# Optimization experiments

Hardware: AMD Instinct MI355X
Metric: run time of the kernel (lower is better)

The kernel has to match this reference:

```python
import jax, jax.numpy as jnp
import numpy as np

M = 16
WIDTH = 9 * M  # 144, hardcoded width_G=9 in original __init__
N_NODES = 100000
E = 1000000
DEPTH = 3


def setup_inputs() -> dict:
    key = jax.random.key(0)
    ks = jax.random.split(key, 16)
    inp = {}
    inp["score"] = jax.random.normal(ks[0], (N_NODES, 1), dtype=jnp.float32)
    inp["label_idx"] = jax.random.randint(ks[1], (E, 2 * M), 0, N_NODES, dtype=jnp.int64)
    s = 1.0 / np.sqrt(2 * M)
    inp["W_start"] = jax.random.uniform(ks[2], (2 * M, WIDTH), jnp.float32, -s, s)
    inp["b_start"] = jax.random.uniform(ks[3], (WIDTH,), jnp.float32, -s, s)
    sh = 1.0 / np.sqrt(WIDTH)
    for i in range(DEPTH):
        inp[f"W_h{i}"] = jax.random.uniform(ks[4 + 2 * i], (WIDTH, WIDTH), jnp.float32, -sh, sh)
        inp[f"b_h{i}"] = jax.random.uniform(ks[5 + 2 * i], (WIDTH,), jnp.float32, -sh, sh)
    inp["W_end"] = jax.random.uniform(ks[10], (WIDTH, 1), jnp.float32, -sh, sh)
    inp["b_end"] = jax.random.uniform(ks[11], (1,), jnp.float32, -sh, sh)
    return inp


def reference(score, label_idx, W_start, b_start, W_h0, b_h0, W_h1, b_h1, W_h2, b_h2, W_end, b_end):
    # Gather: score is [N,1]; score[label_idx] -> [E, 2M, 1] -> [E, 2M]
    node_input = score[label_idx, 0]  # [E, 2M]
    x = jax.nn.relu(node_input @ W_start + b_start)  # [E, 9M]
    for W, b in ((W_h0, b_h0), (W_h1, b_h1), (W_h2, b_h2)):
        x = jax.nn.relu(x @ W + b)
    return x @ W_end + b_end  # [E, 1]
```

## Files before the change

kernel.cpp:

```cpp
#include <hip/hip_runtime.h>

#define EPW 64
#define NTH 64
#define STRIDE 168

using f32x4 = __attribute__((ext_vector_type(4))) float;
using bf8   = __attribute__((ext_vector_type(8))) short;

__device__ __forceinline__ ushort f2bf(float f) {
    union { float f; unsigned u; } c{f};
    unsigned u = c.u;
    return (ushort)((u + 0x7fffu + ((u >> 16) & 1u)) >> 16);
}

__device__ __forceinline__ unsigned cvt_pk_bf16(float lo, float hi) {
    unsigned r;
    asm("v_cvt_pk_bf16_f32 %0, %1, %2" : "=v"(r) : "v"(lo), "v"(hi));
    return r;
}

__global__ void repack_kernel(const float* __restrict__ Wstart,
                              const float* __restrict__ Wh0,
                              const float* __restrict__ Wh1,
                              const float* __restrict__ Wh2,
                              ushort* __restrict__ frag) {
    int i = blockIdx.x * blockDim.x + threadIdx.x;
    if (i < 4608) {
        int j = i & 7, l = (i >> 3) & 63, nt = i >> 9;
        int k = ((l >> 4) << 3) + j;
        int n = nt * 16 + (l & 15);
        frag[i] = f2bf(Wstart[k * 144 + n]);
    } else if (i < 73728) {
        int r = i - 4608;
        int h = r / 23040; r %= 23040;
        const float* W = (h == 0) ? Wh0 : ((h == 1) ? Wh1 : Wh2);
        int j = r & 7, l = (r >> 3) & 63, rem = r >> 9;
        int ks = rem % 5, nt = rem / 5;
        int k = ks * 32 + ((l >> 4) << 3) + j;
        int n = nt * 16 + (l & 15);
        float v = (k < 144) ? W[k * 144 + n] : 0.0f;
        frag[i] = f2bf(v);
    }
}

template<int KS, bool FINAL>
__device__ __forceinline__ void layer_w(const ushort* __restrict__ wfrag,
                                        const float* __restrict__ bias,
                                        ushort (*act)[STRIDE],
                                        const float* __restrict__ W_end,
                                        float* part, int lane) {
    const int grp = lane >> 4, er = lane & 15;
    bf8 xf[4][KS];
    #pragma unroll
    for (int t = 0; t < 4; t++)
        #pragma unroll
        for (int k = 0; k < KS; k++)
            xf[t][k] = *(const bf8*)&act[t * 16 + er][k * 32 + grp * 8];

    bf8 wc[KS], wn[KS];
    #pragma unroll
    for (int k = 0; k < KS; k++)
        wc[k] = *(const bf8*)&wfrag[((k << 6) + lane) << 3];

    #pragma unroll
    for (int nt = 0; nt < 9; nt++) {
        if (nt < 8) {
            #pragma unroll
            for (int k = 0; k < KS; k++)
                wn[k] = *(const bf8*)&wfrag[((((nt + 1) * KS + k) << 6) + lane) << 3];
        }
        f32x4 bv;
        {
            float4 b4 = *(const float4*)&bias[nt * 16 + grp * 4];
            bv[0] = b4.x; bv[1] = b4.y; bv[2] = b4.z; bv[3] = b4.w;
        }
        f32x4 acc[4] = {bv, bv, bv, bv};
        #pragma unroll
        for (int k = 0; k < KS; k++)
            #pragma unroll
            for (int t = 0; t < 4; t++)
                acc[t] = __builtin_amdgcn_mfma_f32_16x16x32_bf16(wc[k], xf[t][k], acc[t], 0, 0, 0);

        if constexpr (FINAL) {
            float4 wv = *(const float4*)&W_end[nt * 16 + grp * 4];
            #pragma unroll
            for (int t = 0; t < 4; t++)
                part[t] += fmaxf(acc[t][0], 0.f) * wv.x + fmaxf(acc[t][1], 0.f) * wv.y
                         + fmaxf(acc[t][2], 0.f) * wv.z + fmaxf(acc[t][3], 0.f) * wv.w;
        } else {
            #pragma unroll
            for (int t = 0; t < 4; t++) {
                uint2 o;
                o.x = cvt_pk_bf16(fmaxf(acc[t][0], 0.f), fmaxf(acc[t][1], 0.f));
                o.y = cvt_pk_bf16(fmaxf(acc[t][2], 0.f), fmaxf(acc[t][3], 0.f));
                *(uint2*)&act[t * 16 + er][nt * 16 + grp * 4] = o;
            }
        }
        #pragma unroll
        for (int k = 0; k < KS; k++)
            wc[k] = wn[k];
    }
}

__global__ __launch_bounds__(NTH, 2)
void mlp_kernel(const float* __restrict__ score,
                const int* __restrict__ label_idx,
                const float* __restrict__ b_start,
                const float* __restrict__ b_h0,
                const float* __restrict__ b_h1,
                const float* __restrict__ b_h2,
                const float* __restrict__ W_end,
                const float* __restrict__ b_end,
                const ushort* __restrict__ frag,
                float* __restrict__ out) {
    __shared__ ushort act[EPW][STRIDE];
    const int lane = threadIdx.x;
    const long gid = blockIdx.x;

    {
        uint4 z = {0u, 0u, 0u, 0u};
        *(uint4*)&act[lane][144] = z;
        *(uint4*)&act[lane][152] = z;
    }

    const int4* lidx4 = (const int4*)label_idx + gid * 512;
    #pragma unroll
    for (int q = 0; q < 8; q++) {
        int p = q * 64 + lane;
        int4 v = lidx4[p];
        float f0 = score[v.x], f1 = score[v.y], f2 = score[v.z], f3 = score[v.w];
        uint2 o;
        o.x = cvt_pk_bf16(f0, f1);
        o.y = cvt_pk_bf16(f2, f3);
        *(uint2*)&act[p >> 3][(p & 7) << 2] = o;
    }

    float part[4] = {0.f, 0.f, 0.f, 0.f};
    layer_w<1, false>(frag,                 b_start, act, nullptr, part, lane);
    layer_w<5, false>(frag + 4608,          b_h0,    act, nullptr, part, lane);
    layer_w<5, false>(frag + 4608 + 23040,  b_h1,    act, nullptr, part, lane);
    layer_w<5, true >(frag + 4608 + 46080,  b_h2,    act, W_end,   part, lane);

    #pragma unroll
    for (int t = 0; t < 4; t++) {
        part[t] += __shfl_xor(part[t], 16, 64);
        part[t] += __shfl_xor(part[t], 32, 64);
    }
    if (lane < 16) {
        float be = b_end[0];
        #pragma unroll
        for (int t = 0; t < 4; t++)
            out[gid * EPW + t * 16 + lane] = be + part[t];
    }
}

extern "C" void kernel_launch(void* const* d_in, const int* in_sizes, int n_in,
                              void* d_out, int out_size, void* d_ws, size_t ws_size,
                              hipStream_t stream) {
    const float* score   = (const float*)d_in[0];
    const int*   lidx    = (const int*)  d_in[1];
    const float* W_start = (const float*)d_in[2];
    const float* b_start = (const float*)d_in[3];
    const float* W_h0    = (const float*)d_in[4];
    const float* b_h0    = (const float*)d_in[5];
    const float* W_h1    = (const float*)d_in[6];
    const float* b_h1    = (const float*)d_in[7];
    const float* W_h2    = (const float*)d_in[8];
    const float* b_h2    = (const float*)d_in[9];
    const float* W_end   = (const float*)d_in[10];
    const float* b_end   = (const float*)d_in[11];
    float* out = (float*)d_out;

    ushort* frag = (ushort*)d_ws;

    const int n_edges = in_sizes[1] / 32;

    repack_kernel<<<288, 256, 0, stream>>>(W_start, W_h0, W_h1, W_h2, frag);

    mlp_kernel<<<n_edges / EPW, NTH, 0, stream>>>(score, lidx, b_start, b_h0, b_h1, b_h2,
                                                  W_end, b_end, frag, out);
}
```

Measured before the change: 218.5 us.

## Split each layer's output tiles across two waves per block

Moves from one wave per 64-edge block to two waves. Each wave loads the full activation fragments, then computes its own subset of the nine output column tiles, with barriers between layers and a shared-memory reduction for the final dot product. The weight-prefetch double buffer is dropped. This halves the serial MFMA chain per wave and doubles wave-level parallelism per block, at the cost of duplicated activation loads, extra __syncthreads, and an uneven 5/4 tile split.

Result: slower. 489.7 us (+124.1%).

```diff
diff --git a/kernel.cpp b/kernel.cpp
--- a/kernel.cpp
+++ b/kernel.cpp
@@ -1,7 +1,7 @@
 #include <hip/hip_runtime.h>
 
 #define EPW 64
-#define NTH 64
+#define NTH 128
 #define STRIDE 168
 
 using f32x4 = __attribute__((ext_vector_type(4))) float;
@@ -43,32 +43,20 @@
     }
 }
 
-template<int KS, bool FINAL>
-__device__ __forceinline__ void layer_w(const ushort* __restrict__ wfrag,
-                                        const float* __restrict__ bias,
-                                        ushort (*act)[STRIDE],
-                                        const float* __restrict__ W_end,
-                                        float* part, int lane) {
+template<int KS, int NTB, int NTE, bool FINAL>
+__device__ __forceinline__ void compute_nts(const ushort* __restrict__ wfrag,
+                                            const float* __restrict__ bias,
+                                            ushort (*act)[STRIDE],
+                                            const float* __restrict__ W_end,
+                                            const bf8 (*xf)[KS],
+                                            float* part, int lane) {
     const int grp = lane >> 4, er = lane & 15;
-    bf8 xf[4][KS];
     #pragma unroll
-    for (int t = 0; t < 4; t++)
+    for (int nt = NTB; nt < NTE; nt++) {
+        bf8 wf5[KS];
         #pragma unroll
         for (int k = 0; k < KS; k++)
-            xf[t][k] = *(const bf8*)&act[t * 16 + er][k * 32 + grp * 8];
-
-    bf8 wc[KS], wn[KS];
-    #pragma unroll
-    for (int k = 0; k < KS; k++)
-        wc[k] = *(const bf8*)&wfrag[((k << 6) + lane) << 3];
-
-    #pragma unroll
-    for (int nt = 0; nt < 9; nt++) {
-        if (nt < 8) {
-            #pragma unroll
-            for (int k = 0; k < KS; k++)
-                wn[k] = *(const bf8*)&wfrag[((((nt + 1) * KS + k) << 6) + lane) << 3];
-        }
+            wf5[k] = *(const bf8*)&wfrag[(((nt * KS + k) << 6) + lane) << 3];
         f32x4 bv;
         {
             float4 b4 = *(const float4*)&bias[nt * 16 + grp * 4];
@@ -79,7 +67,7 @@
         for (int k = 0; k < KS; k++)
             #pragma unroll
             for (int t = 0; t < 4; t++)
-                acc[t] = __builtin_amdgcn_mfma_f32_16x16x32_bf16(wc[k], xf[t][k], acc[t], 0, 0, 0);
+                acc[t] = __builtin_amdgcn_mfma_f32_16x16x32_bf16(wf5[k], xf[t][k], acc[t], 0, 0, 0);
 
         if constexpr (FINAL) {
             float4 wv = *(const float4*)&W_end[nt * 16 + grp * 4];
@@ -96,13 +84,32 @@
                 *(uint2*)&act[t * 16 + er][nt * 16 + grp * 4] = o;
             }
         }
+    }
+}
+
+template<int KS, bool FINAL>
+__device__ __forceinline__ void layer_w(const ushort* __restrict__ wfrag,
+                                        const float* __restrict__ bias,
+                                        ushort (*act)[STRIDE],
+                                        const float* __restrict__ W_end,
+                                        float* part, int wave, int lane) {
+    const int grp = lane >> 4, er = lane & 15;
+    bf8 xf[4][KS];
+    #pragma unroll
+    for (int t = 0; t < 4; t++)
         #pragma unroll
         for (int k = 0; k < KS; k++)
-            wc[k] = wn[k];
-    }
-}
-
-__global__ __launch_bounds__(NTH, 2)
+            xf[t][k] = *(const bf8*)&act[t * 16 + er][k * 32 + grp * 8];
+    __syncthreads();
+
+    if (wave == 0)
+        compute_nts<KS, 0, 5, FINAL>(wfrag, bias, act, W_end, xf, part, lane);
+    else
+        compute_nts<KS, 5, 9, FINAL>(wfrag, bias, act, W_end, xf, part, lane);
+    __syncthreads();
+}
+
+__global__ __launch_bounds__(NTH, 4)
 void mlp_kernel(const float* __restrict__ score,
                 const int* __restrict__ label_idx,
                 const float* __restrict__ b_start,
@@ -114,19 +121,21 @@
                 const ushort* __restrict__ frag,
                 float* __restrict__ out) {
     __shared__ ushort act[EPW][STRIDE];
-    const int lane = threadIdx.x;
+    __shared__ float pdot[2 * EPW];
+    const int tid = threadIdx.x;
+    const int lane = tid & 63;
+    const int wave = tid >> 6;
     const long gid = blockIdx.x;
 
     {
         uint4 z = {0u, 0u, 0u, 0u};
-        *(uint4*)&act[lane][144] = z;
-        *(uint4*)&act[lane][152] = z;
+        *(uint4*)&act[tid >> 1][144 + ((tid & 1) << 3)] = z;
     }
 
     const int4* lidx4 = (const int4*)label_idx + gid * 512;
     #pragma unroll
-    for (int q = 0; q < 8; q++) {
-        int p = q * 64 + lane;
+    for (int q = 0; q < 4; q++) {
+        int p = q * 128 + tid;
         int4 v = lidx4[p];
         float f0 = score[v.x], f1 = score[v.y], f2 = score[v.z], f3 = score[v.w];
         uint2 o;
@@ -134,24 +143,39 @@
         o.y = cvt_pk_bf16(f2, f3);
         *(uint2*)&act[p >> 3][(p & 7) << 2] = o;
     }
+    __syncthreads();
 
     float part[4] = {0.f, 0.f, 0.f, 0.f};
-    layer_w<1, false>(frag,                 b_start, act, nullptr, part, lane);
-    layer_w<5, false>(frag + 4608,          b_h0,    act, nullptr, part, lane);
-    layer_w<5, false>(frag + 4608 + 23040,  b_h1,    act, nullptr, part, lane);
-    layer_w<5, true >(frag + 4608 + 46080,  b_h2,    act, W_end,   part, lane);
-
-    #pragma unroll
-    for (int t = 0; t < 4; t++) {
-        part[t] += __shfl_xor(part[t], 16, 64);
-        part[t] += __shfl_xor(part[t], 32, 64);
-    }
-    if (lane < 16) {
-        float be = b_end[0];
+    layer_w<1, false>(frag,                 b_start, act, nullptr, part, wave, lane);
+    layer_w<5, false>(frag + 4608,          b_h0,    act, nullptr, part, wave, lane);
+    layer_w<5, false>(frag + 4608 + 23040,  b_h1,    act, nullptr, part, wave, lane);
+    {
+        const int grp = lane >> 4, er = lane & 15;
+        bf8 xf[4][5];
         #pragma unroll
         for (int t = 0; t < 4; t++)
-            out[gid * EPW + t * 16 + lane] = be + part[t];
-    }
+            #pragma unroll
+            for (int k = 0; k < 5; k++)
+                xf[t][k] = *(const bf8*)&act[t * 16 + er][k * 32 + grp * 8];
+        __syncthreads();
+        if (wave == 0)
+            compute_nts<5, 0, 5, true>(frag + 4608 + 46080, b_h2, act, W_end, xf, part, lane);
+        else
+            compute_nts<5, 5, 9, true>(frag + 4608 + 46080, b_h2, act, W_end, xf, part, lane);
+        #pragma unroll
+        for (int t = 0; t < 4; t++) {
+            part[t] += __shfl_xor(part[t], 16, 64);
+            part[t] += __shfl_xor(part[t], 32, 64);
+        }
+        if (lane < 16) {
+            #pragma unroll
+            for (int t = 0; t < 4; t++)
+                pdot[wave * EPW + t * 16 + lane] = part[t];
+        }
+        __syncthreads();
+    }
+    if (tid < EPW)
+        out[gid * EPW + tid] = b_end[0] + pdot[tid] + pdot[EPW + tid];
 }
 
 extern "C" void kernel_launch(void* const* d_in, const int* in_sizes, int n_in,
```
